# Kernel optimization log

Measured on AMD Instinct MI355X. Metric: run time of the kernel, lower is better.

The kernel has to match this reference:

```python
import jax, jax.numpy as jnp
import numpy as np

NUM_HEADS = 16
LN_EPS = 1e-5


def _layer_norm(x, g, b):
    m = x.mean(-1, keepdims=True)
    v = x.var(-1, keepdims=True)
    return (x - m) / jnp.sqrt(v + LN_EPS) * g + b


def setup_inputs() -> dict:
    key = jax.random.key(0)
    ks = jax.random.split(key, 4)
    Bq, Bk, Nk, C = 128, 128, 256, 1024
    return {
        "qx": jax.random.normal(ks[0], (Bq, 1, C), jnp.float32),
        "kx": jax.random.normal(ks[1], (Bk, Nk, C), jnp.float32),
        "gq": jnp.ones((C,), jnp.float32),
        "bq": jnp.zeros((C,), jnp.float32),
        "gk": jnp.ones((C,), jnp.float32),
        "bk": jnp.zeros((C,), jnp.float32),
        "Wq": jax.random.normal(ks[2], (C, C), jnp.float32) * (C ** -0.5),
        "Wk": jax.random.normal(ks[3], (C, C), jnp.float32) * (C ** -0.5),
    }


def reference(qx, kx, gq, bq, gk, bk, Wq, Wk):
    H = NUM_HEADS
    Bq, _, C = qx.shape  # qx: [Bq, 1, C]
    Bk, Nk, _ = kx.shape  # kx: [Bk, Nk, C]
    hd = C // H
    scale = hd ** -0.5
    # LayerNorm + linear projections (nn.Linear: x @ W.T, no bias)
    q = (_layer_norm(qx, gq, bq) @ Wq.T).reshape(Bq, H, hd)       # [Bq, H, hd] (Nq=1 squeezed)
    k = (_layer_norm(kx, gk, bk) @ Wk.T).reshape(Bk, Nk, H, hd)   # [Bk, Nk, H, hd]
    # Full bipartite cross-batch attention scores: [Bq, Bk, H, Nk]
    attn = jnp.einsum('qhc,knhc->qkhn', q, k) * scale
    attn = jax.nn.softmax(attn, axis=-1)
    # v = kx broadcast over heads in original einsum 'khnc,qkhn->qkc';
    # equivalent: sum attn over heads, then contract over Nk.
    w = attn.sum(axis=2)                                           # [Bq, Bk, Nk]
    x = jnp.einsum('knc,qkn->qkc', kx, w)                          # [Bq, Bk, C]
    return x
```

## Files before the change

### kernel.cpp

```cpp
#include <hip/hip_runtime.h>


typedef unsigned short ushort_t;
typedef __bf16 bf16x8 __attribute__((ext_vector_type(8)));
typedef float f32x4 __attribute__((ext_vector_type(4)));

#define AS1 __attribute__((address_space(1)))
#define AS3 __attribute__((address_space(3)))

__device__ __forceinline__ void gload_lds16(const void* g, void* l) {
  __builtin_amdgcn_global_load_lds((const AS1 unsigned int*)g, (AS3 unsigned int*)l, 16, 0, 0);
}

__device__ __forceinline__ ushort_t f2bf(float f) {
  unsigned u = __float_as_uint(f);
  unsigned r = u + 0x7FFFu + ((u >> 16) & 1u);
  return (ushort_t)(r >> 16);
}

__global__ __launch_bounds__(256) void cvt_bf16_kernel(const float* __restrict__ src,
                                                       ushort_t* __restrict__ dst, int n4) {
  int i = blockIdx.x * 256 + threadIdx.x;
  if (i < n4) {
    float4 v = ((const float4*)src)[i];
    ushort4 o;
    o.x = f2bf(v.x); o.y = f2bf(v.y); o.z = f2bf(v.z); o.w = f2bf(v.w);
    ((ushort4*)dst)[i] = o;
  }
}

__global__ __launch_bounds__(256) void ln_kernel(const float* __restrict__ kx,
                                                 const float* __restrict__ qx,
                                                 const float* __restrict__ gk,
                                                 const float* __restrict__ bk,
                                                 const float* __restrict__ gq,
                                                 const float* __restrict__ bq,
                                                 ushort_t* __restrict__ kln,
                                                 ushort_t* __restrict__ qln) {
  int row = blockIdx.x;
  const float* src; ushort_t* dst; const float* g; const float* bb;
  if (row < 32768) {
    src = kx + (size_t)row * 1024; dst = kln + (size_t)row * 1024; g = gk; bb = bk;
  } else {
    int r = row - 32768;
    src = qx + (size_t)r * 1024; dst = qln + (size_t)r * 1024; g = gq; bb = bq;
  }
  int tid = threadIdx.x;
  float4 v = ((const float4*)src)[tid];
  float s  = v.x + v.y + v.z + v.w;
  float s2 = v.x*v.x + v.y*v.y + v.z*v.z + v.w*v.w;
  #pragma unroll
  for (int off = 1; off < 64; off <<= 1) {
    s  += __shfl_xor(s, off);
    s2 += __shfl_xor(s2, off);
  }
  __shared__ float red[8];
  int wid = tid >> 6, lane = tid & 63;
  if (lane == 0) { red[wid] = s; red[4 + wid] = s2; }
  __syncthreads();
  s  = red[0] + red[1] + red[2] + red[3];
  s2 = red[4] + red[5] + red[6] + red[7];
  float mean = s * (1.0f / 1024.0f);
  float var  = s2 * (1.0f / 1024.0f) - mean * mean;
  float rstd = rsqrtf(var + 1e-5f);
  float4 gg = ((const float4*)g)[tid];
  float4 b4 = ((const float4*)bb)[tid];
  ushort4 o;
  o.x = f2bf((v.x - mean) * rstd * gg.x + b4.x);
  o.y = f2bf((v.y - mean) * rstd * gg.y + b4.y);
  o.z = f2bf((v.z - mean) * rstd * gg.z + b4.z);
  o.w = f2bf((v.w - mean) * rstd * gg.w + b4.w);
  ((ushort4*)dst)[tid] = o;
}

__global__ __launch_bounds__(512, 2) void gemm256_kernel(const ushort_t* __restrict__ A,
                                                         const ushort_t* __restrict__ Bt,
                                                         ushort_t* __restrict__ Cpk,
                                                         const ushort_t* __restrict__ qA,
                                                         const ushort_t* __restrict__ qB,
                                                         ushort_t* __restrict__ qC,
                                                         int M, int N) {
  __shared__ ushort_t lds[4][2][256 * 32];

  const int tid = threadIdx.x, lane = tid & 63, wid = tid >> 6;
  const int g = lane >> 4, rr = lane & 15;

  if (blockIdx.x >= 512) {
    const bool act = (tid < 256);
    ushort_t* AsQ = &lds[0][0][0];
    ushort_t* BsQ = AsQ + 2 * 128 * 32;
    const int nt = blockIdx.x - 512;
    const size_t n0 = (size_t)nt * 128;

    const int rlo = lane >> 2;
    const int cl  = lane & 3;
    const int wr = wid >> 1, wc = wid & 1;

    f32x4 acc[4][4];
    #pragma unroll
    for (int i = 0; i < 4; ++i)
      #pragma unroll
      for (int j = 0; j < 4; ++j) acc[i][j] = (f32x4){0.f, 0.f, 0.f, 0.f};

    if (act) {
      #pragma unroll
      for (int c = 0; c < 2; ++c) {
        int row = (wid << 5) + (c << 4) + rlo;
        int gch = cl ^ (row & 3);
        gload_lds16(qA + (size_t)row * 1024 + gch * 8, AsQ + ((wid << 5) + (c << 4)) * 32);
        gload_lds16(qB + (n0 + row) * 1024 + gch * 8, BsQ + ((wid << 5) + (c << 4)) * 32);
      }
    }

    for (int t = 0; t < 32; ++t) {
      __syncthreads();
      if (act) {
        if (t + 1 < 32) {
          int k0 = (t + 1) * 32;
          #pragma unroll
          for (int c = 0; c < 2; ++c) {
            int row = (wid << 5) + (c << 4) + rlo;
            int gch = cl ^ (row & 3);
            gload_lds16(qA + (size_t)row * 1024 + k0 + gch * 8,
                        AsQ + ((t + 1) & 1) * 4096 + ((wid << 5) + (c << 4)) * 32);
            gload_lds16(qB + (n0 + row) * 1024 + k0 + gch * 8,
                        BsQ + ((t + 1) & 1) * 4096 + ((wid << 5) + (c << 4)) * 32);
          }
        }
        const ushort_t* as = AsQ + (t & 1) * 4096;
        const ushort_t* bs = BsQ + (t & 1) * 4096;
        bf16x8 af[4], bfr[4];
        #pragma unroll
        for (int i = 0; i < 4; ++i) {
          int rowA = (wr << 6) + (i << 4) + rr;
          af[i] = *(const bf16x8*)&as[rowA * 32 + (g ^ (rowA & 3)) * 8];
          int rowB = (wc << 6) + (i << 4) + rr;
          bfr[i] = *(const bf16x8*)&bs[rowB * 32 + (g ^ (rowB & 3)) * 8];
        }
        #pragma unroll
        for (int i = 0; i < 4; ++i)
          #pragma unroll
          for (int j = 0; j < 4; ++j)
            acc[i][j] = __builtin_amdgcn_mfma_f32_16x16x32_bf16(af[i], bfr[j], acc[i][j], 0, 0, 0);
      }
    }

    if (act) {
      #pragma unroll
      for (int i = 0; i < 4; ++i)
        #pragma unroll
        for (int j = 0; j < 4; ++j)
          #pragma unroll
          for (int rg = 0; rg < 4; ++rg) {
            size_t row = (wr << 6) + (i << 4) + (g << 2) + rg;
            size_t col = n0 + (wc << 6) + (j << 4) + rr;
            qC[row * 1024 + col] = f2bf(acc[i][j][rg]);
          }
    }
    return;
  }

  const int wr = wid >> 2, wc = wid & 3;

  const int Mt = M >> 8, Nt = N >> 8;
  const int nwg = Mt * Nt;
  const int qq = nwg >> 3, r8 = nwg & 7;
  const int xcd = blockIdx.x & 7, idx = blockIdx.x >> 3;
  const int wg = (xcd < r8 ? xcd * (qq + 1) : r8 * (qq + 1) + (xcd - r8) * qq) + idx;
  const int mt = wg / Nt, nt = wg - mt * Nt;
  const size_t m0 = (size_t)mt << 8, n0 = (size_t)nt << 8;

  const int s_r  = lane >> 2;
  const int s_gr = (lane & 3) ^ (s_r & 3) ^ ((s_r >> 2) & 3);

  const ushort_t* Abase = A  + m0 * 1024;
  const ushort_t* Bbase = Bt + n0 * 1024;

  f32x4 acc[8][4];
  #pragma unroll
  for (int i = 0; i < 8; ++i)
    #pragma unroll
    for (int j = 0; j < 4; ++j) acc[i][j] = (f32x4){0.f, 0.f, 0.f, 0.f};

  auto stageA = [&](int kt) {
    const int k0 = kt << 5;
    ushort_t* dst = &lds[kt & 3][0][0];
    #pragma unroll
    for (int it = 0; it < 2; ++it) {
      int ci = (wid << 1) | it;
      int r  = (ci << 4) + s_r;
      gload_lds16(Abase + (size_t)r * 1024 + k0 + (s_gr << 3), dst + (ci << 9));
    }
  };
  auto stageB = [&](int kt) {
    const int k0 = kt << 5;
    ushort_t* dst = &lds[kt & 3][1][0];
    #pragma unroll
    for (int it = 0; it < 2; ++it) {
      int ci = (wid << 1) | it;
      int r  = (ci << 4) + s_r;
      gload_lds16(Bbase + (size_t)r * 1024 + k0 + (s_gr << 3), dst + (ci << 9));
    }
  };

  stageA(0); stageB(0); stageA(1); stageB(1); stageA(2); stageB(2);
  asm volatile("s_waitcnt vmcnt(8)" ::: "memory");
  __builtin_amdgcn_s_barrier();

  const int rsw = (rr & 3) ^ ((rr >> 2) & 3);

  #pragma unroll 1
  for (int u = 0; u < 29; ++u) {
    const ushort_t* as = &lds[u & 3][0][0];
    const ushort_t* bs = &lds[u & 3][1][0];
    bf16x8 af[8];
    {
      #pragma unroll
      for (int i = 0; i < 8; ++i) {
        int r = (wr << 7) + (i << 4) + rr;
        af[i] = *(const bf16x8*)&as[(r << 5) + ((g ^ rsw) << 3)];
      }
      int r0 = (wc << 6) + rr;
      bf16x8 b0 = *(const bf16x8*)&bs[(r0 << 5) + ((g ^ rsw) << 3)];
      int r1 = (wc << 6) + 16 + rr;
      bf16x8 b1 = *(const bf16x8*)&bs[(r1 << 5) + ((g ^ rsw) << 3)];
      stageA(u + 3);
      __builtin_amdgcn_s_setprio(1);
      #pragma unroll
      for (int i = 0; i < 8; ++i) {
        acc[i][0] = __builtin_amdgcn_mfma_f32_16x16x32_bf16(af[i], b0, acc[i][0], 0, 0, 0);
        acc[i][1] = __builtin_amdgcn_mfma_f32_16x16x32_bf16(af[i], b1, acc[i][1], 0, 0, 0);
      }
      __builtin_amdgcn_s_setprio(0);
      __builtin_amdgcn_s_barrier();
    }
    {
      int r2 = (wc << 6) + 32 + rr;
      bf16x8 b2 = *(const bf16x8*)&bs[(r2 << 5) + ((g ^ rsw) << 3)];
      int r3 = (wc << 6) + 48 + rr;
      bf16x8 b3 = *(const bf16x8*)&bs[(r3 << 5) + ((g ^ rsw) << 3)];
      stageB(u + 3);
      __builtin_amdgcn_s_setprio(1);
      #pragma unroll
      for (int i = 0; i < 8; ++i) {
        acc[i][2] = __builtin_amdgcn_mfma_f32_16x16x32_bf16(af[i], b2, acc[i][2], 0, 0, 0);
        acc[i][3] = __builtin_amdgcn_mfma_f32_16x16x32_bf16(af[i], b3, acc[i][3], 0, 0, 0);
      }
      __builtin_amdgcn_s_setprio(0);
      asm volatile("s_waitcnt vmcnt(8)" ::: "memory");
      __builtin_amdgcn_s_barrier();
    }
  }

  asm volatile("s_waitcnt vmcnt(0)" ::: "memory");
  __builtin_amdgcn_s_barrier();
  #pragma unroll 1
  for (int u = 29; u < 32; ++u) {
    const ushort_t* as = &lds[u & 3][0][0];
    const ushort_t* bs = &lds[u & 3][1][0];
    bf16x8 af2[8], bfj[4];
    #pragma unroll
    for (int i = 0; i < 8; ++i) {
      int r = (wr << 7) + (i << 4) + rr;
      af2[i] = *(const bf16x8*)&as[(r << 5) + ((g ^ rsw) << 3)];
    }
    #pragma unroll
    for (int j = 0; j < 4; ++j) {
      int r = (wc << 6) + (j << 4) + rr;
      bfj[j] = *(const bf16x8*)&bs[(r << 5) + ((g ^ rsw) << 3)];
    }
    #pragma unroll
    for (int i = 0; i < 8; ++i)
      #pragma unroll
      for (int j = 0; j < 4; ++j)
        acc[i][j] = __builtin_amdgcn_mfma_f32_16x16x32_bf16(af2[i], bfj[j], acc[i][j], 0, 0, 0);
  }

  #pragma unroll
  for (int i = 0; i < 8; ++i)
    #pragma unroll
    for (int j = 0; j < 4; ++j)
      #pragma unroll
      for (int rg = 0; rg < 4; ++rg) {
        size_t row = m0 + (wr << 7) + (i << 4) + (g << 2) + rg;
        size_t col = n0 + (wc << 6) + (j << 4) + rr;
        int kb = (int)(row >> 8), t = (int)((row >> 4) & 15), r16 = (int)(row & 15);
        int h = (int)(col >> 6), ch = (int)(col & 63);
        size_t idx = ((((size_t)kb * 16 + h) * 16 + t) << 10)
                   + ((ch >> 5) << 9) + (((ch >> 3) & 3) << 7) + (r16 << 3) + (ch & 7);
        Cpk[idx] = f2bf(acc[i][j][rg]);
      }
}

__global__ __launch_bounds__(256, 3) void scores_kernel(const ushort_t* __restrict__ qp,
                                                        const ushort_t* __restrict__ kpk,
                                                        ushort_t* __restrict__ wbuf) {
  __shared__ float pbuf[2][16][258];

  const int tid = threadIdx.x, lane = tid & 63, wid = tid >> 6;
  const int g = lane >> 4, rr = lane & 15;

  const int b = blockIdx.x;
  const int wg = (b & 7) * 128 + (b >> 3);
  const int kb = wg >> 3;
  const int q0 = (wg & 7) << 4;

  const int hs = wid;

  float w_acc[16][4];
  #pragma unroll
  for (int t = 0; t < 16; ++t)
    #pragma unroll
    for (int r = 0; r < 4; ++r) w_acc[t][r] = 0.f;

  const ushort_t* qrow = qp + (size_t)(q0 + rr) * 1024;
  const ushort_t* kbb  = kpk + ((size_t)kb * 16) * 16384 + g * 128 + rr * 8;

  for (int hp = 0; hp < 4; ++hp) {
    const int h = hp * 4 + hs;
    const int co = h * 64 + g * 8;
    bf16x8 aq0 = *(const bf16x8*)(qrow + co);
    bf16x8 aq1 = *(const bf16x8*)(qrow + co + 32);
    const ushort_t* hb = kbb + (size_t)h * 16384;
    f32x4 s[16];
    #pragma unroll
    for (int t = 0; t < 16; ++t) {
      bf16x8 b0 = *(const bf16x8*)(hb + t * 1024);
      bf16x8 b1 = *(const bf16x8*)(hb + t * 1024 + 512);
      f32x4 a = (f32x4){0.f, 0.f, 0.f, 0.f};
      a = __builtin_amdgcn_mfma_f32_16x16x32_bf16(aq0, b0, a, 0, 0, 0);
      a = __builtin_amdgcn_mfma_f32_16x16x32_bf16(aq1, b1, a, 0, 0, 0);
      s[t] = a;
    }
    #pragma unroll
    for (int r = 0; r < 4; ++r) {
      float mx = s[0][r];
      #pragma unroll
      for (int t = 1; t < 16; ++t) mx = fmaxf(mx, s[t][r]);
      mx = fmaxf(mx, __shfl_xor(mx, 1));
      mx = fmaxf(mx, __shfl_xor(mx, 2));
      mx = fmaxf(mx, __shfl_xor(mx, 4));
      mx = fmaxf(mx, __shfl_xor(mx, 8));
      float sum = 0.f;
      float e[16];
      #pragma unroll
      for (int t = 0; t < 16; ++t) {
        e[t] = __expf((s[t][r] - mx) * 0.125f);
        sum += e[t];
      }
      sum += __shfl_xor(sum, 1);
      sum += __shfl_xor(sum, 2);
      sum += __shfl_xor(sum, 4);
      sum += __shfl_xor(sum, 8);
      float inv = 1.0f / sum;
      #pragma unroll
      for (int t = 0; t < 16; ++t) w_acc[t][r] += e[t] * inv;
    }
  }

  __syncthreads();
  if (hs >= 2) {
    #pragma unroll
    for (int t = 0; t < 16; ++t)
      #pragma unroll
      for (int r = 0; r < 4; ++r)
        pbuf[hs - 2][(g << 2) + r][t * 16 + rr] = w_acc[t][r];
  }
  __syncthreads();
  if (hs < 2) {
    #pragma unroll
    for (int t = 0; t < 16; ++t)
      #pragma unroll
      for (int r = 0; r < 4; ++r)
        w_acc[t][r] += pbuf[hs][(g << 2) + r][t * 16 + rr];
    if (hs == 1) {
      #pragma unroll
      for (int t = 0; t < 16; ++t)
        #pragma unroll
        for (int r = 0; r < 4; ++r)
          pbuf[1][(g << 2) + r][t * 16 + rr] = w_acc[t][r];
    }
  }
  __syncthreads();
  if (hs == 0) {
    ushort_t* wb = wbuf + (size_t)kb * 32768;
    #pragma unroll
    for (int t = 0; t < 16; ++t)
      #pragma unroll
      for (int r = 0; r < 4; ++r) {
        float v = w_acc[t][r] + pbuf[1][(g << 2) + r][t * 16 + rr];
        wb[(size_t)(q0 + (g << 2) + r) * 256 + t * 16 + rr] = f2bf(v);
      }
  }
}

__global__ __launch_bounds__(256, 4) void pv_kernel(const ushort_t* __restrict__ wbuf,
                                                    const float* __restrict__ kx,
                                                    float* __restrict__ xout) {
  const int tid = threadIdx.x, lane = tid & 63, wid = tid >> 6;
  const int g = lane >> 4, rr = lane & 15;

  const int b = blockIdx.x;
  const int wg = (b & 7) * 128 + (b >> 3);
  const int kb = wg >> 3;
  const int c0 = (wg & 7) * 128;

  const int wr = wid >> 1, wc = wid & 1;

  f32x4 acc[4][4];
  #pragma unroll
  for (int i = 0; i < 4; ++i)
    #pragma unroll
    for (int j = 0; j < 4; ++j) acc[i][j] = (f32x4){0.f, 0.f, 0.f, 0.f};

  const ushort_t* wb = wbuf + (size_t)kb * 32768;
  const float* kxb = kx + (size_t)kb * 256 * 1024;

  for (int nc = 0; nc < 8; ++nc) {
    const int n0 = nc * 32 + g * 8;
    bf16x8 af[4];
    #pragma unroll
    for (int i = 0; i < 4; ++i) {
      int q = (wr << 6) + (i << 4) + rr;
      af[i] = *(const bf16x8*)(wb + (size_t)q * 256 + n0);
    }
    #pragma unroll
    for (int j = 0; j < 4; ++j) {
      int c = c0 + (wc << 6) + (j << 4) + rr;
      const float* src = kxb + (size_t)n0 * 1024 + c;
      float f[8];
      #pragma unroll
      for (int jj = 0; jj < 8; ++jj) f[jj] = src[(size_t)jj * 1024];
      bf16x8 bb;
      #pragma unroll
      for (int jj = 0; jj < 8; ++jj) bb[jj] = (__bf16)f[jj];
      #pragma unroll
      for (int i = 0; i < 4; ++i)
        acc[i][j] = __builtin_amdgcn_mfma_f32_16x16x32_bf16(af[i], bb, acc[i][j], 0, 0, 0);
    }
  }

  #pragma unroll
  for (int i = 0; i < 4; ++i)
    #pragma unroll
    for (int j = 0; j < 4; ++j)
      #pragma unroll
      for (int rg = 0; rg < 4; ++rg) {
        int q = (wr << 6) + (i << 4) + (g << 2) + rg;
        int c = c0 + (wc << 6) + (j << 4) + rr;
        xout[((size_t)q * 128 + kb) * 1024 + c] = acc[i][j][rg];
      }
}

extern "C" void kernel_launch(void* const* d_in, const int* in_sizes, int n_in,
                              void* d_out, int out_size, void* d_ws, size_t ws_size,
                              hipStream_t stream) {
  const float* qx = (const float*)d_in[0];
  const float* kx = (const float*)d_in[1];
  const float* gq = (const float*)d_in[2];
  const float* bq = (const float*)d_in[3];
  const float* gk = (const float*)d_in[4];
  const float* bk = (const float*)d_in[5];
  const float* Wq = (const float*)d_in[6];
  const float* Wk = (const float*)d_in[7];

  char* ws = (char*)d_ws;
  ushort_t* kkp   = (ushort_t*)(ws);
  ushort_t* qproj = (ushort_t*)(ws + 67108864);
  ushort_t* wbuf  = (ushort_t*)(ws + 67371008);
  ushort_t* qln   = (ushort_t*)(ws + 67371008);
  ushort_t* Wqb   = (ushort_t*)(ws + 67371008 + 262144);
  ushort_t* Wkb   = (ushort_t*)(ws + 67371008 + 2359296);
  ushort_t* kln  = (ushort_t*)d_out;
  float*    xout = (float*)d_out;

  cvt_bf16_kernel<<<1024, 256, 0, stream>>>(Wq, Wqb, 262144);
  cvt_bf16_kernel<<<1024, 256, 0, stream>>>(Wk, Wkb, 262144);
  ln_kernel<<<32896, 256, 0, stream>>>(kx, qx, gk, bk, gq, bq, kln, qln);
  gemm256_kernel<<<520, 512, 0, stream>>>(kln, Wkb, kkp, qln, Wqb, qproj, 32768, 1024);
  scores_kernel<<<1024, 256, 0, stream>>>(qproj, kkp, wbuf);
  pv_kernel<<<1024, 256, 0, stream>>>(wbuf, kx, xout);
}
```

Measured before the change: 269.8 us.

## Double-buffer main GEMM and fold q-projection tiles into every block's epilogue

The main 256x256 GEMM drops from a 4-stage split A/B pipeline to a 2-stage LDS double buffer. Each k-step now stages A and B together and reloads all fragments, which halves LDS use and raises the launch-bounds occupancy hint to 4. The 8 extra blocks that computed the small q projection are removed. Instead, every one of the 512 blocks computes one 16x16 q-projection tile straight from global memory after its epilogue, so the extra tail wave goes away. Risks: a shallower prefetch pipeline, a simpler XOR swizzle that may cause more LDS bank conflicts, and uncached global reads for the q tiles.

```diff
diff --git a/kernel.cpp b/kernel.cpp
--- a/kernel.cpp
+++ b/kernel.cpp
@@ -73,93 +73,17 @@
   ((ushort4*)dst)[tid] = o;
 }
 
-__global__ __launch_bounds__(512, 2) void gemm256_kernel(const ushort_t* __restrict__ A,
+__global__ __launch_bounds__(512, 4) void gemm256_kernel(const ushort_t* __restrict__ A,
                                                          const ushort_t* __restrict__ Bt,
                                                          ushort_t* __restrict__ Cpk,
                                                          const ushort_t* __restrict__ qA,
                                                          const ushort_t* __restrict__ qB,
                                                          ushort_t* __restrict__ qC,
                                                          int M, int N) {
-  __shared__ ushort_t lds[4][2][256 * 32];
+  __shared__ ushort_t lds[2][2][256 * 32];
 
   const int tid = threadIdx.x, lane = tid & 63, wid = tid >> 6;
   const int g = lane >> 4, rr = lane & 15;
-
-  if (blockIdx.x >= 512) {
-    const bool act = (tid < 256);
-    ushort_t* AsQ = &lds[0][0][0];
-    ushort_t* BsQ = AsQ + 2 * 128 * 32;
-    const int nt = blockIdx.x - 512;
-    const size_t n0 = (size_t)nt * 128;
-
-    const int rlo = lane >> 2;
-    const int cl  = lane & 3;
-    const int wr = wid >> 1, wc = wid & 1;
-
-    f32x4 acc[4][4];
-    #pragma unroll
-    for (int i = 0; i < 4; ++i)
-      #pragma unroll
-      for (int j = 0; j < 4; ++j) acc[i][j] = (f32x4){0.f, 0.f, 0.f, 0.f};
-
-    if (act) {
-      #pragma unroll
-      for (int c = 0; c < 2; ++c) {
-        int row = (wid << 5) + (c << 4) + rlo;
-        int gch = cl ^ (row & 3);
-        gload_lds16(qA + (size_t)row * 1024 + gch * 8, AsQ + ((wid << 5) + (c << 4)) * 32);
-        gload_lds16(qB + (n0 + row) * 1024 + gch * 8, BsQ + ((wid << 5) + (c << 4)) * 32);
-      }
-    }
-
-    for (int t = 0; t < 32; ++t) {
-      __syncthreads();
-      if (act) {
-        if (t + 1 < 32) {
-          int k0 = (t + 1) * 32;
-          #pragma unroll
-          for (int c = 0; c < 2; ++c) {
-            int row = (wid << 5) + (c << 4) + rlo;
-            int gch = cl ^ (row & 3);
-            gload_lds16(qA + (size_t)row * 1024 + k0 + gch * 8,
-                        AsQ + ((t + 1) & 1) * 4096 + ((wid << 5) + (c << 4)) * 32);
-            gload_lds16(qB + (n0 + row) * 1024 + k0 + gch * 8,
-                        BsQ + ((t + 1) & 1) * 4096 + ((wid << 5) + (c << 4)) * 32);
-          }
-        }
-        const ushort_t* as = AsQ + (t & 1) * 4096;
-        const ushort_t* bs = BsQ + (t & 1) * 4096;
-        bf16x8 af[4], bfr[4];
-        #pragma unroll
-        for (int i = 0; i < 4; ++i) {
-          int rowA = (wr << 6) + (i << 4) + rr;
-          af[i] = *(const bf16x8*)&as[rowA * 32 + (g ^ (rowA & 3)) * 8];
-          int rowB = (wc << 6) + (i << 4) + rr;
-          bfr[i] = *(const bf16x8*)&bs[rowB * 32 + (g ^ (rowB & 3)) * 8];
-        }
-        #pragma unroll
-        for (int i = 0; i < 4; ++i)
-          #pragma unroll
-          for (int j = 0; j < 4; ++j)
-            acc[i][j] = __builtin_amdgcn_mfma_f32_16x16x32_bf16(af[i], bfr[j], acc[i][j], 0, 0, 0);
-      }
-    }
-
-    if (act) {
-      #pragma unroll
-      for (int i = 0; i < 4; ++i)
-        #pragma unroll
-        for (int j = 0; j < 4; ++j)
-          #pragma unroll
-          for (int rg = 0; rg < 4; ++rg) {
-            size_t row = (wr << 6) + (i << 4) + (g << 2) + rg;
-            size_t col = n0 + (wc << 6) + (j << 4) + rr;
-            qC[row * 1024 + col] = f2bf(acc[i][j][rg]);
-          }
-    }
-    return;
-  }
-
   const int wr = wid >> 2, wc = wid & 3;
 
   const int Mt = M >> 8, Nt = N >> 8;
@@ -171,7 +95,7 @@
   const size_t m0 = (size_t)mt << 8, n0 = (size_t)nt << 8;
 
   const int s_r  = lane >> 2;
-  const int s_gr = (lane & 3) ^ (s_r & 3) ^ ((s_r >> 2) & 3);
+  const int s_gr = (lane & 3) ^ (s_r & 3);
 
   const ushort_t* Abase = A  + m0 * 1024;
   const ushort_t* Bbase = Bt + n0 * 1024;
@@ -182,98 +106,100 @@
     #pragma unroll
     for (int j = 0; j < 4; ++j) acc[i][j] = (f32x4){0.f, 0.f, 0.f, 0.f};
 
-  auto stageA = [&](int kt) {
+  auto stage = [&](int kt) {
     const int k0 = kt << 5;
-    ushort_t* dst = &lds[kt & 3][0][0];
+    ushort_t* dstA = &lds[kt & 1][0][0];
+    ushort_t* dstB = &lds[kt & 1][1][0];
     #pragma unroll
     for (int it = 0; it < 2; ++it) {
       int ci = (wid << 1) | it;
       int r  = (ci << 4) + s_r;
-      gload_lds16(Abase + (size_t)r * 1024 + k0 + (s_gr << 3), dst + (ci << 9));
-    }
-  };
-  auto stageB = [&](int kt) {
-    const int k0 = kt << 5;
-    ushort_t* dst = &lds[kt & 3][1][0];
+      gload_lds16(Abase + (size_t)r * 1024 + k0 + (s_gr << 3), dstA + (ci << 9));
+    }
     #pragma unroll
     for (int it = 0; it < 2; ++it) {
       int ci = (wid << 1) | it;
       int r  = (ci << 4) + s_r;
-      gload_lds16(Bbase + (size_t)r * 1024 + k0 + (s_gr << 3), dst + (ci << 9));
+      gload_lds16(Bbase + (size_t)r * 1024 + k0 + (s_gr << 3), dstB + (ci << 9));
     }
   };
 
-  stageA(0); stageB(0); stageA(1); stageB(1); stageA(2); stageB(2);
-  asm volatile("s_waitcnt vmcnt(8)" ::: "memory");
+  stage(0); stage(1);
+  asm volatile("s_waitcnt vmcnt(4)" ::: "memory");
   __builtin_amdgcn_s_barrier();
 
-  const int rsw = (rr & 3) ^ ((rr >> 2) & 3);
+  const int rsw = rr & 3;
 
   #pragma unroll 1
-  for (int u = 0; u < 29; ++u) {
-    const ushort_t* as = &lds[u & 3][0][0];
-    const ushort_t* bs = &lds[u & 3][1][0];
-    bf16x8 af[8];
-    {
-      #pragma unroll
-      for (int i = 0; i < 8; ++i) {
-        int r = (wr << 7) + (i << 4) + rr;
-        af[i] = *(const bf16x8*)&as[(r << 5) + ((g ^ rsw) << 3)];
-      }
-      int r0 = (wc << 6) + rr;
-      bf16x8 b0 = *(const bf16x8*)&bs[(r0 << 5) + ((g ^ rsw) << 3)];
-      int r1 = (wc << 6) + 16 + rr;
-      bf16x8 b1 = *(const bf16x8*)&bs[(r1 << 5) + ((g ^ rsw) << 3)];
-      stageA(u + 3);
-      __builtin_amdgcn_s_setprio(1);
-      #pragma unroll
-      for (int i = 0; i < 8; ++i) {
-        acc[i][0] = __builtin_amdgcn_mfma_f32_16x16x32_bf16(af[i], b0, acc[i][0], 0, 0, 0);
-        acc[i][1] = __builtin_amdgcn_mfma_f32_16x16x32_bf16(af[i], b1, acc[i][1], 0, 0, 0);
-      }
-      __builtin_amdgcn_s_setprio(0);
-      __builtin_amdgcn_s_barrier();
-    }
-    {
-      int r2 = (wc << 6) + 32 + rr;
-      bf16x8 b2 = *(const bf16x8*)&bs[(r2 << 5) + ((g ^ rsw) << 3)];
-      int r3 = (wc << 6) + 48 + rr;
-      bf16x8 b3 = *(const bf16x8*)&bs[(r3 << 5) + ((g ^ rsw) << 3)];
-      stageB(u + 3);
-      __builtin_amdgcn_s_setprio(1);
-      #pragma unroll
-      for (int i = 0; i < 8; ++i) {
-        acc[i][2] = __builtin_amdgcn_mfma_f32_16x16x32_bf16(af[i], b2, acc[i][2], 0, 0, 0);
-        acc[i][3] = __builtin_amdgcn_mfma_f32_16x16x32_bf16(af[i], b3, acc[i][3], 0, 0, 0);
-      }
-      __builtin_amdgcn_s_setprio(0);
-      asm volatile("s_waitcnt vmcnt(8)" ::: "memory");
-      __builtin_amdgcn_s_barrier();
-    }
-  }
-
-  asm volatile("s_waitcnt vmcnt(0)" ::: "memory");
-  __builtin_amdgcn_s_barrier();
-  #pragma unroll 1
-  for (int u = 29; u < 32; ++u) {
-    const ushort_t* as = &lds[u & 3][0][0];
-    const ushort_t* bs = &lds[u & 3][1][0];
-    bf16x8 af2[8], bfj[4];
+  for (int u = 0; u < 30; ++u) {
+    const ushort_t* as = &lds[u & 1][0][0];
+    const ushort_t* bs = &lds[u & 1][1][0];
+    bf16x8 af[8], bf[4];
     #pragma unroll
     for (int i = 0; i < 8; ++i) {
       int r = (wr << 7) + (i << 4) + rr;
-      af2[i] = *(const bf16x8*)&as[(r << 5) + ((g ^ rsw) << 3)];
+      af[i] = *(const bf16x8*)&as[(r << 5) + ((g ^ rsw) << 3)];
     }
     #pragma unroll
     for (int j = 0; j < 4; ++j) {
       int r = (wc << 6) + (j << 4) + rr;
-      bfj[j] = *(const bf16x8*)&bs[(r << 5) + ((g ^ rsw) << 3)];
-    }
+      bf[j] = *(const bf16x8*)&bs[(r << 5) + ((g ^ rsw) << 3)];
+    }
+    asm volatile("s_waitcnt lgkmcnt(0)" ::: "memory");
+    __builtin_amdgcn_s_barrier();
+    stage(u + 2);
+    __builtin_amdgcn_s_setprio(1);
     #pragma unroll
     for (int i = 0; i < 8; ++i)
       #pragma unroll
       for (int j = 0; j < 4; ++j)
-        acc[i][j] = __builtin_amdgcn_mfma_f32_16x16x32_bf16(af2[i], bfj[j], acc[i][j], 0, 0, 0);
+        acc[i][j] = __builtin_amdgcn_mfma_f32_16x16x32_bf16(af[i], bf[j], acc[i][j], 0, 0, 0);
+    __builtin_amdgcn_s_setprio(0);
+    asm volatile("s_waitcnt vmcnt(4)" ::: "memory");
+    __builtin_amdgcn_s_barrier();
+  }
+
+  {
+    const ushort_t* as = &lds[0][0][0];
+    const ushort_t* bs = &lds[0][1][0];
+    bf16x8 af[8], bf[4];
+    #pragma unroll
+    for (int i = 0; i < 8; ++i) {
+      int r = (wr << 7) + (i << 4) + rr;
+      af[i] = *(const bf16x8*)&as[(r << 5) + ((g ^ rsw) << 3)];
+    }
+    #pragma unroll
+    for (int j = 0; j < 4; ++j) {
+      int r = (wc << 6) + (j << 4) + rr;
+      bf[j] = *(const bf16x8*)&bs[(r << 5) + ((g ^ rsw) << 3)];
+    }
+    #pragma unroll
+    for (int i = 0; i < 8; ++i)
+      #pragma unroll
+      for (int j = 0; j < 4; ++j)
+        acc[i][j] = __builtin_amdgcn_mfma_f32_16x16x32_bf16(af[i], bf[j], acc[i][j], 0, 0, 0);
+    asm volatile("s_waitcnt vmcnt(0)" ::: "memory");
+    __builtin_amdgcn_s_barrier();
+  }
+  {
+    const ushort_t* as = &lds[1][0][0];
+    const ushort_t* bs = &lds[1][1][0];
+    bf16x8 af[8], bf[4];
+    #pragma unroll
+    for (int i = 0; i < 8; ++i) {
+      int r = (wr << 7) + (i << 4) + rr;
+      af[i] = *(const bf16x8*)&as[(r << 5) + ((g ^ rsw) << 3)];
+    }
+    #pragma unroll
+    for (int j = 0; j < 4; ++j) {
+      int r = (wc << 6) + (j << 4) + rr;
+      bf[j] = *(const bf16x8*)&bs[(r << 5) + ((g ^ rsw) << 3)];
+    }
+    #pragma unroll
+    for (int i = 0; i < 8; ++i)
+      #pragma unroll
+      for (int j = 0; j < 4; ++j)
+        acc[i][j] = __builtin_amdgcn_mfma_f32_16x16x32_bf16(af[i], bf[j], acc[i][j], 0, 0, 0);
   }
 
   #pragma unroll
@@ -290,6 +216,22 @@
                    + ((ch >> 5) << 9) + (((ch >> 3) & 3) << 7) + (r16 << 3) + (ch & 7);
         Cpk[idx] = f2bf(acc[i][j][rg]);
       }
+
+  {
+    const int mq = wg >> 6, nq = wg & 63;
+    const ushort_t* qa = qA + (size_t)(mq * 16 + rr) * 1024 + g * 8;
+    const ushort_t* qb = qB + (size_t)(nq * 16 + rr) * 1024 + g * 8;
+    f32x4 qacc = (f32x4){0.f, 0.f, 0.f, 0.f};
+    #pragma unroll
+    for (int kk = 0; kk < 32; ++kk) {
+      bf16x8 a = *(const bf16x8*)(qa + kk * 32);
+      bf16x8 b = *(const bf16x8*)(qb + kk * 32);
+      qacc = __builtin_amdgcn_mfma_f32_16x16x32_bf16(a, b, qacc, 0, 0, 0);
+    }
+    #pragma unroll
+    for (int rg = 0; rg < 4; ++rg)
+      qC[(size_t)(mq * 16 + (g << 2) + rg) * 1024 + nq * 16 + rr] = f2bf(qacc[rg]);
+  }
 }
 
 __global__ __launch_bounds__(256, 3) void scores_kernel(const ushort_t* __restrict__ qp,
@@ -477,7 +419,7 @@
   cvt_bf16_kernel<<<1024, 256, 0, stream>>>(Wq, Wqb, 262144);
   cvt_bf16_kernel<<<1024, 256, 0, stream>>>(Wk, Wkb, 262144);
   ln_kernel<<<32896, 256, 0, stream>>>(kx, qx, gk, bk, gq, bq, kln, qln);
-  gemm256_kernel<<<520, 512, 0, stream>>>(kln, Wkb, kkp, qln, Wqb, qproj, 32768, 1024);
+  gemm256_kernel<<<512, 512, 0, stream>>>(kln, Wkb, kkp, qln, Wqb, qproj, 32768, 1024);
   scores_kernel<<<1024, 256, 0, stream>>>(qproj, kkp, wbuf);
   pv_kernel<<<1024, 256, 0, stream>>>(wbuf, kx, xout);
 }
```

Result: slower. 933.1 us (+245.8%).

## Fold Q projection into K-projection GEMM blocks and simplify LDS swizzle

Applied to the files above, without the earlier changes.

Removes the 8 extra dedicated Q-projection workgroups appended to the GEMM launch. Instead, each of the 512 main blocks computes one 16x16 tile of the Q projection after its K tile, using MFMA operands loaded directly from global memory. The goal is to eliminate a tail wave of blocks that ran beyond the 512 co-resident slots. It also simplifies the LDS XOR swizzle from two levels to one, which may change the bank-conflict behaviour of the main GEMM. All 8 waves in each block compute and write the same Q tile, so that small piece of work is done redundantly.

```diff
diff --git a/kernel.cpp b/kernel.cpp
--- a/kernel.cpp
+++ b/kernel.cpp
@@ -84,82 +84,6 @@
 
   const int tid = threadIdx.x, lane = tid & 63, wid = tid >> 6;
   const int g = lane >> 4, rr = lane & 15;
-
-  if (blockIdx.x >= 512) {
-    const bool act = (tid < 256);
-    ushort_t* AsQ = &lds[0][0][0];
-    ushort_t* BsQ = AsQ + 2 * 128 * 32;
-    const int nt = blockIdx.x - 512;
-    const size_t n0 = (size_t)nt * 128;
-
-    const int rlo = lane >> 2;
-    const int cl  = lane & 3;
-    const int wr = wid >> 1, wc = wid & 1;
-
-    f32x4 acc[4][4];
-    #pragma unroll
-    for (int i = 0; i < 4; ++i)
-      #pragma unroll
-      for (int j = 0; j < 4; ++j) acc[i][j] = (f32x4){0.f, 0.f, 0.f, 0.f};
-
-    if (act) {
-      #pragma unroll
-      for (int c = 0; c < 2; ++c) {
-        int row = (wid << 5) + (c << 4) + rlo;
-        int gch = cl ^ (row & 3);
-        gload_lds16(qA + (size_t)row * 1024 + gch * 8, AsQ + ((wid << 5) + (c << 4)) * 32);
-        gload_lds16(qB + (n0 + row) * 1024 + gch * 8, BsQ + ((wid << 5) + (c << 4)) * 32);
-      }
-    }
-
-    for (int t = 0; t < 32; ++t) {
-      __syncthreads();
-      if (act) {
-        if (t + 1 < 32) {
-          int k0 = (t + 1) * 32;
-          #pragma unroll
-          for (int c = 0; c < 2; ++c) {
-            int row = (wid << 5) + (c << 4) + rlo;
-            int gch = cl ^ (row & 3);
-            gload_lds16(qA + (size_t)row * 1024 + k0 + gch * 8,
-                        AsQ + ((t + 1) & 1) * 4096 + ((wid << 5) + (c << 4)) * 32);
-            gload_lds16(qB + (n0 + row) * 1024 + k0 + gch * 8,
-                        BsQ + ((t + 1) & 1) * 4096 + ((wid << 5) + (c << 4)) * 32);
-          }
-        }
-        const ushort_t* as = AsQ + (t & 1) * 4096;
-        const ushort_t* bs = BsQ + (t & 1) * 4096;
-        bf16x8 af[4], bfr[4];
-        #pragma unroll
-        for (int i = 0; i < 4; ++i) {
-          int rowA = (wr << 6) + (i << 4) + rr;
-          af[i] = *(const bf16x8*)&as[rowA * 32 + (g ^ (rowA & 3)) * 8];
-          int rowB = (wc << 6) + (i << 4) + rr;
-          bfr[i] = *(const bf16x8*)&bs[rowB * 32 + (g ^ (rowB & 3)) * 8];
-        }
-        #pragma unroll
-        for (int i = 0; i < 4; ++i)
-          #pragma unroll
-          for (int j = 0; j < 4; ++j)
-            acc[i][j] = __builtin_amdgcn_mfma_f32_16x16x32_bf16(af[i], bfr[j], acc[i][j], 0, 0, 0);
-      }
-    }
-
-    if (act) {
-      #pragma unroll
-      for (int i = 0; i < 4; ++i)
-        #pragma unroll
-        for (int j = 0; j < 4; ++j)
-          #pragma unroll
-          for (int rg = 0; rg < 4; ++rg) {
-            size_t row = (wr << 6) + (i << 4) + (g << 2) + rg;
-            size_t col = n0 + (wc << 6) + (j << 4) + rr;
-            qC[row * 1024 + col] = f2bf(acc[i][j][rg]);
-          }
-    }
-    return;
-  }
-
   const int wr = wid >> 2, wc = wid & 3;
 
   const int Mt = M >> 8, Nt = N >> 8;
@@ -171,7 +95,7 @@
   const size_t m0 = (size_t)mt << 8, n0 = (size_t)nt << 8;
 
   const int s_r  = lane >> 2;
-  const int s_gr = (lane & 3) ^ (s_r & 3) ^ ((s_r >> 2) & 3);
+  const int s_gr = (lane & 3) ^ (s_r & 3);
 
   const ushort_t* Abase = A  + m0 * 1024;
   const ushort_t* Bbase = Bt + n0 * 1024;
@@ -207,7 +131,7 @@
   asm volatile("s_waitcnt vmcnt(8)" ::: "memory");
   __builtin_amdgcn_s_barrier();
 
-  const int rsw = (rr & 3) ^ ((rr >> 2) & 3);
+  const int rsw = rr & 3;
 
   #pragma unroll 1
   for (int u = 0; u < 29; ++u) {
@@ -290,6 +214,22 @@
                    + ((ch >> 5) << 9) + (((ch >> 3) & 3) << 7) + (r16 << 3) + (ch & 7);
         Cpk[idx] = f2bf(acc[i][j][rg]);
       }
+
+  {
+    const int mq = wg >> 6, nq = wg & 63;
+    const ushort_t* qa = qA + (size_t)(mq * 16 + rr) * 1024 + g * 8;
+    const ushort_t* qb = qB + (size_t)(nq * 16 + rr) * 1024 + g * 8;
+    f32x4 qacc = (f32x4){0.f, 0.f, 0.f, 0.f};
+    #pragma unroll
+    for (int kk = 0; kk < 32; ++kk) {
+      bf16x8 a = *(const bf16x8*)(qa + kk * 32);
+      bf16x8 b = *(const bf16x8*)(qb + kk * 32);
+      qacc = __builtin_amdgcn_mfma_f32_16x16x32_bf16(a, b, qacc, 0, 0, 0);
+    }
+    #pragma unroll
+    for (int rg = 0; rg < 4; ++rg)
+      qC[(size_t)(mq * 16 + (g << 2) + rg) * 1024 + nq * 16 + rr] = f2bf(qacc[rg]);
+  }
 }
 
 __global__ __launch_bounds__(256, 3) void scores_kernel(const ushort_t* __restrict__ qp,
@@ -477,7 +417,7 @@
   cvt_bf16_kernel<<<1024, 256, 0, stream>>>(Wq, Wqb, 262144);
   cvt_bf16_kernel<<<1024, 256, 0, stream>>>(Wk, Wkb, 262144);
   ln_kernel<<<32896, 256, 0, stream>>>(kx, qx, gk, bk, gq, bq, kln, qln);
-  gemm256_kernel<<<520, 512, 0, stream>>>(kln, Wkb, kkp, qln, Wqb, qproj, 32768, 1024);
+  gemm256_kernel<<<512, 512, 0, stream>>>(kln, Wkb, kkp, qln, Wqb, qproj, 32768, 1024);
   scores_kernel<<<1024, 256, 0, stream>>>(qproj, kkp, wbuf);
   pv_kernel<<<1024, 256, 0, stream>>>(wbuf, kx, xout);
 }
```

After: 280.7 us. +4.0%, slower.
